# Kernel tuning notes

Hardware: AMD Instinct MI355X
Metric: run time of the kernel (lower is better)

The kernel has to match this reference:

```python
import jax, jax.numpy as jnp
import numpy as np

# GConvLSTM (torch_geometric_temporal) single step, H=None,C=None -> zeros.
# Each gate g uses two ChebConvs: conv_x_g(X) + conv_h_g(H) + (w_c_g*C for i,f; only i,f,o have w_c) + b_g
# With H=C=0: gate preact = conv_x_g(X) + conv_h_g(0) + b_g. ChebConv(0)=0 only if bias=False;
# torch_geometric_temporal ChebConvs use bias=True by default, so conv_h_g(0) = bias_h_g (a vector).
# We fold conv_h bias into b. Cheb recursion with sym norm, lambda_max=2 default in ChebConv? Actually
# ChebConv requires lambda_max or normalization='sym' default uses lambda_max=2.0 assumption:
# Tx_0 = x; Tx_1 = L_hat @ x where L_hat = -D^-1/2 A D^-1/2 (since L_scaled = L - I = -A_norm for lambda_max=2);
# Tx_k = 2*L_hat@Tx_{k-1} - Tx_{k-2}. out = sum_k Tx_k @ W_k + bias.

MULT = 2
IN_CH = 10
WIDTHS = [8 * MULT, 16 * MULT, 32 * MULT, 76 * MULT]
KS = [2, 3, 4, 5]
NUM_CLASSES = 2
N_NODES = 100000
N_EDGES = 3200000


def _norm_adj(edge_index, n):
    src, dst = edge_index[0], edge_index[1]
    deg = jax.ops.segment_sum(jnp.ones_like(src, dtype=jnp.float32), dst, num_segments=n)
    dinv = jnp.where(deg > 0, jax.lax.rsqrt(jnp.maximum(deg, 1.0)), 0.0)
    w = dinv[src] * dinv[dst]  # [E]
    return src, dst, w


def _lhat_mul(x, src, dst, w, n):
    # L_hat @ x = -A_norm @ x  (lambda_max=2, sym norm, no self loops added in scaled L beyond -I cancel)
    msg = x[src] * w[:, None]  # [E,F]
    agg = jax.ops.segment_sum(msg, dst, num_segments=n)
    return -agg


def cheb_conv(x, Ws, b, src, dst, w, n):
    # Ws: [K, F_in, F_out]
    K = Ws.shape[0]
    Tx0 = x
    out = Tx0 @ Ws[0]
    if K > 1:
        Tx1 = _lhat_mul(Tx0, src, dst, w, n)
        out = out + Tx1 @ Ws[1]
        for k in range(2, K):
            Tx2 = 2.0 * _lhat_mul(Tx1, src, dst, w, n) - Tx0
            out = out + Tx2 @ Ws[k]
            Tx0, Tx1 = Tx1, Tx2
    return out + b


def gconv_lstm_step(x, params, src, dst, w, n):
    # params: dict with per-gate Wx,Wh (cheb weights), bx,bh, b, and w_ci,w_cf,w_co
    def conv_pair(g):
        cx = cheb_conv(x, params[f'Wx_{g}'], params[f'bx_{g}'], src, dst, w, n)
        # H = 0 => conv_h contributes only its bias
        return cx + params[f'bh_{g}'] + params[f'b_{g}']
    # C = 0 => peephole terms w_c*C vanish
    i = jax.nn.sigmoid(conv_pair('i'))
    f = jax.nn.sigmoid(conv_pair('f'))
    c = i * jnp.tanh(conv_pair('c'))
    o = jax.nn.sigmoid(conv_pair('o'))
    h = o * jnp.tanh(c)
    return h


def _make_layer_params(key, f_in, f_out, K):
    p = {}
    ks = jax.random.split(key, 16)
    scale = 1.0 / np.sqrt(f_in * K)
    for gi, g in enumerate(['i', 'f', 'c', 'o']):
        p[f'Wx_{g}'] = jax.random.normal(ks[4 * gi], (K, f_in, f_out), jnp.float32) * scale
        p[f'bx_{g}'] = jnp.zeros((f_out,), jnp.float32)
        p[f'bh_{g}'] = jnp.zeros((f_out,), jnp.float32)
        p[f'b_{g}'] = jnp.zeros((f_out,), jnp.float32)
    return p


def setup_inputs() -> dict:
    key = jax.random.key(0)
    kx, ke, kp, kl = jax.random.split(key, 4)
    x = jax.random.normal(kx, (N_NODES, IN_CH), jnp.float32)
    edge_index = jax.random.randint(ke, (2, N_EDGES), 0, N_NODES, dtype=jnp.int64)
    layer_keys = jax.random.split(kp, 4)
    params = []
    f_in = IN_CH
    for li, (f_out, K) in enumerate(zip(WIDTHS, KS)):
        params.append(_make_layer_params(layer_keys[li], f_in, f_out, K))
        f_in = f_out
    flat = {}
    for li, p in enumerate(params):
        for k, v in p.items():
            flat[f'l{li}_{k}'] = v
    kw, kb = jax.random.split(kl)
    flat['lin_W'] = jax.random.normal(kw, (WIDTHS[-1], NUM_CLASSES), jnp.float32) * (1.0 / np.sqrt(WIDTHS[-1]))
    flat['lin_b'] = jnp.zeros((NUM_CLASSES,), jnp.float32)
    return {'x': x, 'edge_index': edge_index, **flat}


_GATE_KEYS = [f'{pre}_{g}' for g in ['i', 'f', 'c', 'o'] for pre in ['Wx', 'bx', 'bh', 'b']]


def _forward(x, edge_index, params_by_layer, lin_W, lin_b):
    n = x.shape[0]
    src, dst, w = _norm_adj(edge_index, n)
    h = x
    for p in params_by_layer:
        h = gconv_lstm_step(h, p, src, dst, w, n)
        h = jax.nn.relu(h)  # dropout: eval mode -> identity
    logits = h @ lin_W + lin_b
    return jax.nn.softmax(logits, axis=-1)


def reference(x, edge_index,
              l0_Wx_i, l0_bx_i, l0_bh_i, l0_b_i, l0_Wx_f, l0_bx_f, l0_bh_f, l0_b_f, l0_Wx_c, l0_bx_c, l0_bh_c, l0_b_c, l0_Wx_o, l0_bx_o, l0_bh_o, l0_b_o,
              l1_Wx_i, l1_bx_i, l1_bh_i, l1_b_i, l1_Wx_f, l1_bx_f, l1_bh_f, l1_b_f, l1_Wx_c, l1_bx_c, l1_bh_c, l1_b_c, l1_Wx_o, l1_bx_o, l1_bh_o, l1_b_o,
              l2_Wx_i, l2_bx_i, l2_bh_i, l2_b_i, l2_Wx_f, l2_bx_f, l2_bh_f, l2_b_f, l2_Wx_c, l2_bx_c, l2_bh_c, l2_b_c, l2_Wx_o, l2_bx_o, l2_bh_o, l2_b_o,
              l3_Wx_i, l3_bx_i, l3_bh_i, l3_b_i, l3_Wx_f, l3_bx_f, l3_bh_f, l3_b_f, l3_Wx_c, l3_bx_c, l3_bh_c, l3_b_c, l3_Wx_o, l3_bx_o, l3_bh_o, l3_b_o,
              lin_W, lin_b):
    loc = locals()
    params_by_layer = []
    for li in range(4):
        params_by_layer.append({k: loc[f'l{li}_{k}'] for k in _GATE_KEYS})
    return _forward(x, edge_index, params_by_layer, lin_W, lin_b)
```

## Files before the change

### kernel.cpp

```cpp
#include <hip/hip_runtime.h>


#define IN_CH 10
typedef unsigned short u16;
typedef unsigned long long u64;
typedef short bf16x8 __attribute__((ext_vector_type(8)));
typedef float f32x4 __attribute__((ext_vector_type(4)));

struct __align__(8) Edge { int s; float w; };

__device__ __forceinline__ float bf2f(u16 u) { return __uint_as_float(((unsigned)u) << 16); }
__device__ __forceinline__ float lo16f(unsigned v) { return __uint_as_float(v << 16); }
__device__ __forceinline__ float hi16f(unsigned v) { return __uint_as_float(v & 0xffff0000u); }
__device__ __forceinline__ u16 f2bf(float f) {
    unsigned x = __float_as_uint(f);
    return (u16)((x + 0x7fff + ((x >> 16) & 1)) >> 16);
}
__device__ __forceinline__ float ldv(const float* p) { return *p; }
__device__ __forceinline__ float ldv(const u16* p) { return bf2f(*p); }
__device__ __forceinline__ void stv(float* p, float v) { *p = v; }
__device__ __forceinline__ void stv(u16* p, float v) { *p = f2bf(v); }


__global__ void k_count(const int* __restrict__ dst, int* __restrict__ cnt, int e) {
    int i = blockIdx.x * 256 + threadIdx.x;
    if (i < e) atomicAdd(&cnt[dst[i]], 1);
}

__global__ void k_dinv(const int* __restrict__ cnt, float* __restrict__ dinv, int n) {
    int i = blockIdx.x * 256 + threadIdx.x;
    if (i < n) dinv[i] = cnt[i] > 0 ? rsqrtf((float)cnt[i]) : 0.f;
}


__global__ void k_bsum(const int* __restrict__ cnt, int* __restrict__ bsum, int n) {
    __shared__ int red[256];
    int t = threadIdx.x;
    int idx = blockIdx.x * 1024 + t * 4;
    int s = 0;
#pragma unroll
    for (int j = 0; j < 4; j++) s += (idx + j < n) ? cnt[idx + j] : 0;
    red[t] = s;
    __syncthreads();
    for (int off = 128; off > 0; off >>= 1) {
        if (t < off) red[t] += red[t + off];
        __syncthreads();
    }
    if (t == 0) bsum[blockIdx.x] = red[0];
}

__global__ __launch_bounds__(1024) void k_bscan(const int* __restrict__ bsum,
                                                int* __restrict__ boff,
                                                int* __restrict__ total_out, int B) {
    __shared__ int sh[1024];
    int t = threadIdx.x;
    int v = t < B ? bsum[t] : 0;
    sh[t] = v;
    __syncthreads();
    for (int off = 1; off < 1024; off <<= 1) {
        int x = (t >= off) ? sh[t - off] : 0;
        __syncthreads();
        sh[t] += x;
        __syncthreads();
    }
    if (t < B) boff[t] = sh[t] - v;
    if (t == B - 1) *total_out = sh[t];
}

__global__ void k_write(const int* __restrict__ cnt, const int* __restrict__ boff,
                        int* __restrict__ row_ptr, int* __restrict__ cursor, int n) {
    __shared__ int tsum[256];
    int t = threadIdx.x;
    int idx = blockIdx.x * 1024 + t * 4;
    int c[4];
    int s = 0;
#pragma unroll
    for (int j = 0; j < 4; j++) {
        c[j] = (idx + j < n) ? cnt[idx + j] : 0;
        s += c[j];
    }
    tsum[t] = s;
    __syncthreads();
    for (int off = 1; off < 256; off <<= 1) {
        int x = (t >= off) ? tsum[t - off] : 0;
        __syncthreads();
        tsum[t] += x;
        __syncthreads();
    }
    int run = boff[blockIdx.x] + tsum[t] - s;
#pragma unroll
    for (int j = 0; j < 4; j++) {
        if (idx + j < n) {
            row_ptr[idx + j] = run;
            cursor[idx + j] = run;
            run += c[j];
        }
    }
}

__global__ void k_fill(const int* __restrict__ src, const int* __restrict__ dst,
                       const float* __restrict__ dinv, int* __restrict__ cursor,
                       Edge* __restrict__ ed, int e, int dlo, int dhi) {
    int i = blockIdx.x * 256 + threadIdx.x;
    if (i >= e) return;
    int d = dst[i];
    if (d < dlo || d >= dhi) return;
    int s = src[i];
    int pos = atomicAdd(&cursor[d], 1);
    float w = dinv[s] * dinv[d];
    u64 v = (u64)(unsigned)s | ((u64)__float_as_uint(w) << 32);
    *(u64*)&ed[pos] = v;
}


template <int F>
__global__ void k_spmv(const u16* __restrict__ X, const u16* __restrict__ Tprev,
                       u16* __restrict__ Tout, const int* __restrict__ row_ptr,
                       const Edge* __restrict__ ed, int n, float scale) {
    int lane = threadIdx.x;
    int node = blockIdx.x * blockDim.y + threadIdx.y;
    if (node >= n) return;
    int lo = row_ptr[node], hi = row_ptr[node + 1];
    const u16* Xc = X + 2 * lane;
    float a0[4] = {0.f, 0.f, 0.f, 0.f};
    float a1[4] = {0.f, 0.f, 0.f, 0.f};
    int e = lo;
    for (; e + 8 <= hi; e += 8) {
        Edge q[8];
#pragma unroll
        for (int j = 0; j < 8; j++) q[j] = ed[e + j];
        unsigned v[8];
#pragma unroll
        for (int j = 0; j < 8; j++)
            v[j] = *(const unsigned*)(Xc + (size_t)q[j].s * F);
#pragma unroll
        for (int j = 0; j < 8; j++) {
            a0[j & 3] = fmaf(q[j].w, lo16f(v[j]), a0[j & 3]);
            a1[j & 3] = fmaf(q[j].w, hi16f(v[j]), a1[j & 3]);
        }
    }
    for (; e + 4 <= hi; e += 4) {
        Edge q[4];
#pragma unroll
        for (int j = 0; j < 4; j++) q[j] = ed[e + j];
        unsigned v[4];
#pragma unroll
        for (int j = 0; j < 4; j++)
            v[j] = *(const unsigned*)(Xc + (size_t)q[j].s * F);
#pragma unroll
        for (int j = 0; j < 4; j++) {
            a0[j] = fmaf(q[j].w, lo16f(v[j]), a0[j]);
            a1[j] = fmaf(q[j].w, hi16f(v[j]), a1[j]);
        }
    }
    for (; e < hi; e++) {
        Edge q = ed[e];
        unsigned v = *(const unsigned*)(Xc + (size_t)q.s * F);
        a0[0] = fmaf(q.w, lo16f(v), a0[0]);
        a1[0] = fmaf(q.w, hi16f(v), a1[0]);
    }
    float v0 = -scale * ((a0[0] + a0[1]) + (a0[2] + a0[3]));
    float v1 = -scale * ((a1[0] + a1[1]) + (a1[2] + a1[3]));
    if (Tprev) {
        unsigned pv = *(const unsigned*)(Tprev + (size_t)node * F + 2 * lane);
        v0 -= lo16f(pv);
        v1 -= hi16f(pv);
    }
    *(unsigned*)(Tout + (size_t)node * F + 2 * lane) =
        (unsigned)f2bf(v0) | ((unsigned)f2bf(v1) << 16);
}

struct TP { const void* p[5]; };

template <typename ST, int FIN, int K>
__global__ __launch_bounds__(256) void k_chebgate(TP tp, const float* __restrict__ Wp,
                                                  const float* __restrict__ b4,
                                                  ST* __restrict__ H, int n, int F,
                                                  int F4pad) {
    __shared__ float As[FIN][68];
    __shared__ float Ws[FIN][128];
    const int tid = threadIdx.x;
    const int fx = tid & 31, ry = tid >> 5;
    const int row0 = blockIdx.y * 64;
    const int f0 = blockIdx.x * 32;
    const int f = f0 + fx;

    float acc[8][3];
    const float4 bv = *(const float4*)&b4[(size_t)f * 4];
#pragma unroll
    for (int r = 0; r < 8; r++) { acc[r][0] = bv.x; acc[r][1] = bv.y; acc[r][2] = bv.z; }

#pragma unroll
    for (int t = 0; t < K; t++) {
        const ST* T = (const ST*)tp.p[t];
        for (int idx = tid; idx < 64 * FIN; idx += 256) {
            int r = idx / FIN, a = idx - r * FIN;
            int rr = row0 + r;
            if (rr >= n) rr = n - 1;
            As[a][r] = ldv(&T[(size_t)rr * FIN + a]);
        }
        const float* Wt = Wp + (size_t)t * FIN * F4pad + (size_t)f0 * 4;
        for (int idx = tid; idx < FIN * 128; idx += 256) {
            int aa = idx >> 7, c = idx & 127;
            Ws[aa][c] = Wt[(size_t)aa * F4pad + c];
        }
        __syncthreads();
#pragma unroll 2
        for (int a = 0; a < FIN; a++) {
            const float4 w = *(const float4*)&Ws[a][fx * 4];
            const float4 x0 = *(const float4*)&As[a][ry * 8];
            const float4 x1 = *(const float4*)&As[a][ry * 8 + 4];
            const float xr[8] = {x0.x, x0.y, x0.z, x0.w, x1.x, x1.y, x1.z, x1.w};
#pragma unroll
            for (int r = 0; r < 8; r++) {
                acc[r][0] = fmaf(xr[r], w.x, acc[r][0]);
                acc[r][1] = fmaf(xr[r], w.y, acc[r][1]);
                acc[r][2] = fmaf(xr[r], w.z, acc[r][2]);
            }
        }
        __syncthreads();
    }

    if (f < F) {
#pragma unroll
        for (int r = 0; r < 8; r++) {
            int row = row0 + ry * 8 + r;
            if (row < n) {
                float gi = 1.f / (1.f + __expf(-acc[r][0]));
                float go = 1.f / (1.f + __expf(-acc[r][2]));
                float c = gi * tanhf(acc[r][1]);
                float h = go * tanhf(c);
                stv(&H[(size_t)row * F + f], fmaxf(h, 0.f));
            }
        }
    }
}


template <int FIN, int K, int FPAD, int NT>
__global__ __launch_bounds__(256) void k_chebgate_mfma(TP tp, const u16* __restrict__ Wt,
                                                       const float* __restrict__ b3,
                                                       u16* __restrict__ H, int n, int F,
                                                       int Hstride) {
    constexpr int KT = K * FIN;
    const int xb = blockIdx.x / NT;
    const int yb = blockIdx.x % NT;
    const int wave = threadIdx.x >> 6;
    const int lane = threadIdx.x & 63;
    const int r0 = xb * 128 + wave * 32;
    const int f0 = yb * 32;
    const int ln = lane & 15;
    const int lk = lane >> 4;

    f32x4 acc[2][2][3];
#pragma unroll
    for (int rt = 0; rt < 2; rt++)
#pragma unroll
        for (int s = 0; s < 2; s++)
#pragma unroll
            for (int g = 0; g < 3; g++) acc[rt][s][g] = (f32x4){0.f, 0.f, 0.f, 0.f};

    int arow[2];
#pragma unroll
    for (int rt = 0; rt < 2; rt++) {
        int row = r0 + rt * 16 + ln;
        arow[rt] = row < n ? row : n - 1;
    }

    for (int k0 = 0; k0 < KT; k0 += 32) {
        const int t = k0 / FIN;
        const int a0 = k0 % FIN;
        const u16* T = (const u16*)tp.p[t];
        bf16x8 af[2];
#pragma unroll
        for (int rt = 0; rt < 2; rt++)
            af[rt] = *(const bf16x8*)(T + (size_t)arow[rt] * FIN + a0 + lk * 8);
#pragma unroll
        for (int s = 0; s < 2; s++) {
#pragma unroll
            for (int g = 0; g < 3; g++) {
                int col = g * FPAD + f0 + s * 16 + ln;
                bf16x8 bf = *(const bf16x8*)(Wt + (size_t)col * KT + k0 + lk * 8);
#pragma unroll
                for (int rt = 0; rt < 2; rt++)
                    acc[rt][s][g] = __builtin_amdgcn_mfma_f32_16x16x32_bf16(
                        af[rt], bf, acc[rt][s][g], 0, 0, 0);
            }
        }
    }

#pragma unroll
    for (int s = 0; s < 2; s++) {
        int fcol = f0 + s * 16 + ln;
        if (fcol >= F) continue;
        float bi = b3[0 * FPAD + fcol];
        float bc = b3[1 * FPAD + fcol];
        float bo = b3[2 * FPAD + fcol];
#pragma unroll
        for (int rt = 0; rt < 2; rt++) {
#pragma unroll
            for (int reg = 0; reg < 4; reg++) {
                int row = r0 + rt * 16 + lk * 4 + reg;
                if (row < n) {
                    float gi = 1.f / (1.f + __expf(-(acc[rt][s][0][reg] + bi)));
                    float go = 1.f / (1.f + __expf(-(acc[rt][s][2][reg] + bo)));
                    float c = gi * tanhf(acc[rt][s][1][reg] + bc);
                    float h = go * tanhf(c);
                    H[(size_t)row * Hstride + fcol] = f2bf(fmaxf(h, 0.f));
                }
            }
        }
    }
}


template <int FIN, int K, int FPAD, int NT>
__global__ __launch_bounds__(256) void k_chebgate_mfma_fused(
    TP tp, const u16* __restrict__ Wt, const float* __restrict__ b3,
    const float* __restrict__ W2, float* __restrict__ part, int n, int F) {
    constexpr int KT = K * FIN;
    const int xb = blockIdx.x / NT;
    const int yb = blockIdx.x % NT;
    const int wave = threadIdx.x >> 6;
    const int lane = threadIdx.x & 63;
    const int r0 = xb * 128 + wave * 32;
    const int f0 = yb * 32;
    const int ln = lane & 15;
    const int lk = lane >> 4;

    f32x4 acc[2][2][3];
#pragma unroll
    for (int rt = 0; rt < 2; rt++)
#pragma unroll
        for (int s = 0; s < 2; s++)
#pragma unroll
            for (int g = 0; g < 3; g++) acc[rt][s][g] = (f32x4){0.f, 0.f, 0.f, 0.f};

    int arow[2];
#pragma unroll
    for (int rt = 0; rt < 2; rt++) {
        int row = r0 + rt * 16 + ln;
        arow[rt] = row < n ? row : n - 1;
    }

    for (int k0 = 0; k0 < KT; k0 += 32) {
        const int t = k0 / FIN;
        const int a0 = k0 % FIN;
        const u16* T = (const u16*)tp.p[t];
        bf16x8 af[2];
#pragma unroll
        for (int rt = 0; rt < 2; rt++)
            af[rt] = *(const bf16x8*)(T + (size_t)arow[rt] * FIN + a0 + lk * 8);
#pragma unroll
        for (int s = 0; s < 2; s++) {
#pragma unroll
            for (int g = 0; g < 3; g++) {
                int col = g * FPAD + f0 + s * 16 + ln;
                bf16x8 bf = *(const bf16x8*)(Wt + (size_t)col * KT + k0 + lk * 8);
#pragma unroll
                for (int rt = 0; rt < 2; rt++)
                    acc[rt][s][g] = __builtin_amdgcn_mfma_f32_16x16x32_bf16(
                        af[rt], bf, acc[rt][s][g], 0, 0, 0);
            }
        }
    }

    float p0[2][4], p1[2][4];
#pragma unroll
    for (int rt = 0; rt < 2; rt++)
#pragma unroll
        for (int reg = 0; reg < 4; reg++) { p0[rt][reg] = 0.f; p1[rt][reg] = 0.f; }

#pragma unroll
    for (int s = 0; s < 2; s++) {
        int fcol = f0 + s * 16 + ln;
        float w20 = fcol < F ? W2[fcol * 2 + 0] : 0.f;
        float w21 = fcol < F ? W2[fcol * 2 + 1] : 0.f;
        float bi = b3[0 * FPAD + fcol];
        float bc = b3[1 * FPAD + fcol];
        float bo = b3[2 * FPAD + fcol];
#pragma unroll
        for (int rt = 0; rt < 2; rt++) {
#pragma unroll
            for (int reg = 0; reg < 4; reg++) {
                float gi = 1.f / (1.f + __expf(-(acc[rt][s][0][reg] + bi)));
                float go = 1.f / (1.f + __expf(-(acc[rt][s][2][reg] + bo)));
                float c = gi * tanhf(acc[rt][s][1][reg] + bc);
                float h = fmaxf(go * tanhf(c), 0.f);
                p0[rt][reg] = fmaf(h, w20, p0[rt][reg]);
                p1[rt][reg] = fmaf(h, w21, p1[rt][reg]);
            }
        }
    }

#pragma unroll
    for (int rt = 0; rt < 2; rt++) {
#pragma unroll
        for (int reg = 0; reg < 4; reg++) {
            float v0 = p0[rt][reg], v1 = p1[rt][reg];
#pragma unroll
            for (int m = 1; m <= 8; m <<= 1) {
                v0 += __shfl_xor(v0, m);
                v1 += __shfl_xor(v1, m);
            }
            p0[rt][reg] = v0;
            p1[rt][reg] = v1;
        }
    }

    if (ln == 0) {
#pragma unroll
        for (int rt = 0; rt < 2; rt++) {
#pragma unroll
            for (int reg = 0; reg < 4; reg++) {
                int row = r0 + rt * 16 + lk * 4 + reg;
                if (row < n) {
                    float* pp = part + ((size_t)yb * n + row) * 2;
                    pp[0] = p0[rt][reg];
                    pp[1] = p1[rt][reg];
                }
            }
        }
    }
}

__global__ void k_smax(const float* __restrict__ part, const float* __restrict__ b,
                       float* __restrict__ out, int n, int ntiles) {
    int i = blockIdx.x * 256 + threadIdx.x;
    if (i >= n) return;
    float l0 = b[0], l1 = b[1];
    for (int t = 0; t < ntiles; t++) {
        const float* pp = part + ((size_t)t * n + i) * 2;
        l0 += pp[0];
        l1 += pp[1];
    }
    float m = fmaxf(l0, l1);
    float e0 = __expf(l0 - m), e1 = __expf(l1 - m);
    float s = 1.f / (e0 + e1);
    out[(size_t)i * 2 + 0] = e0 * s;
    out[(size_t)i * 2 + 1] = e1 * s;
}


__global__ void k_pack_w(const float* __restrict__ Wi, const float* __restrict__ Wc,
                         const float* __restrict__ Wo, float* __restrict__ Wp,
                         int KFIN, int F, int F4pad) {
    int idx = blockIdx.x * 256 + threadIdx.x;
    int tot = KFIN * F4pad;
    if (idx >= tot) return;
    int c = idx % F4pad;
    int ka = idx / F4pad;
    int f = c >> 2, g = c & 3;
    float v = 0.f;
    if (g < 3 && f < F) {
        const float* Wg = (g == 0) ? Wi : ((g == 1) ? Wc : Wo);
        v = Wg[(size_t)ka * F + f];
    }
    Wp[idx] = v;
}

__global__ void k_pack_b(const float* __restrict__ bxi, const float* __restrict__ bhi,
                         const float* __restrict__ bi, const float* __restrict__ bxc,
                         const float* __restrict__ bhc, const float* __restrict__ bc,
                         const float* __restrict__ bxo, const float* __restrict__ bho,
                         const float* __restrict__ bo, float* __restrict__ b4,
                         int F, int F4pad) {
    int idx = blockIdx.x * 256 + threadIdx.x;
    if (idx >= F4pad) return;
    int f = idx >> 2, g = idx & 3;
    float v = 0.f;
    if (g < 3 && f < F) {
        if (g == 0) v = bxi[f] + bhi[f] + bi[f];
        else if (g == 1) v = bxc[f] + bhc[f] + bc[f];
        else v = bxo[f] + bho[f] + bo[f];
    }
    b4[idx] = v;
}

__global__ void k_pack_wt(const float* __restrict__ Wi, const float* __restrict__ Wc,
                          const float* __restrict__ Wo, u16* __restrict__ Wt,
                          int KT, int Fin, int F, int FPAD) {
    int idx = blockIdx.x * 256 + threadIdx.x;
    int tot = 3 * FPAD * KT;
    if (idx >= tot) return;
    int k = idx % KT;
    int col = idx / KT;
    int g = col / FPAD, f = col % FPAD;
    int t = k / Fin, a = k % Fin;
    float v = 0.f;
    if (f < F) {
        const float* Wg = (g == 0) ? Wi : ((g == 1) ? Wc : Wo);
        v = Wg[((size_t)t * Fin + a) * F + f];
    }
    Wt[idx] = f2bf(v);
}

__global__ void k_pack_b3(const float* __restrict__ bxi, const float* __restrict__ bhi,
                          const float* __restrict__ bi, const float* __restrict__ bxc,
                          const float* __restrict__ bhc, const float* __restrict__ bc,
                          const float* __restrict__ bxo, const float* __restrict__ bho,
                          const float* __restrict__ bo, float* __restrict__ b3,
                          int F, int FPAD) {
    int idx = blockIdx.x * 256 + threadIdx.x;
    if (idx >= 3 * FPAD) return;
    int g = idx / FPAD, f = idx % FPAD;
    float v = 0.f;
    if (f < F) {
        if (g == 0) v = bxi[f] + bhi[f] + bi[f];
        else if (g == 1) v = bxc[f] + bhc[f] + bc[f];
        else v = bxo[f] + bho[f] + bo[f];
    }
    b3[idx] = v;
}

__global__ void k_cvt(const float* __restrict__ x, u16* __restrict__ y, int n) {
    int i = blockIdx.x * 256 + threadIdx.x;
    if (i < n) y[i] = f2bf(x[i]);
}


static inline size_t al(size_t x) { return (x + 255) & ~(size_t)255; }

extern "C" void kernel_launch(void* const* d_in, const int* in_sizes, int n_in,
                              void* d_out, int out_size, void* d_ws, size_t ws_size,
                              hipStream_t stream) {
    const float* X0 = (const float*)d_in[0];
    const int* ei = (const int*)d_in[1];
    const int N = in_sizes[0] / IN_CH;
    const int E = in_sizes[1] / 2;
    const int* src = ei;
    const int* dst = ei + E;

    char* p = (char*)d_ws;
    size_t off = 0;
    auto carve = [&](size_t bytes) -> char* { char* r = p + off; off += al(bytes); return r; };
    int* row_ptr  = (int*)carve((size_t)(N + 1) * 4);
    int* cnt      = (int*)carve((size_t)N * 4);
    int* cursor   = (int*)carve((size_t)N * 4);
    float* dinv   = (float*)carve((size_t)N * 4);
    int* bsum     = (int*)carve((size_t)1024 * 4);
    int* boff     = (int*)carve((size_t)1024 * 4);
    Edge* edges   = (Edge*)carve((size_t)E * 8);
    const size_t S64 = al((size_t)N * 64 * 2);
    char* bufA    = carve(5 * S64);
    char* bufB    = carve((size_t)N * 304);
    float* Wp     = (float*)carve((size_t)48 * 128 * 4);
    float* b4     = (float*)carve((size_t)128 * 4);
    u16* Wt       = (u16*)carve((size_t)480 * 320 * 2);
    float* b3     = (float*)carve((size_t)480 * 4);
    (void)ws_size;

    u16* X0c  = (u16*)bufA;
    u16* T0_1 = (u16*)(bufA + al((size_t)N * 20));
    u16* H0   = (u16*)(bufA + S64);
    u16* T1_1 = (u16*)(bufA + S64 + al((size_t)N * 32));
    u16* T1_2 = (u16*)(bufA + S64 + 2 * al((size_t)N * 32));
    u16* L2T[4];
    for (int t = 0; t < 4; t++) L2T[t] = (u16*)(bufB + t * al((size_t)N * 64));
    u16* L3T[5];
    for (int t = 0; t < 5; t++) L3T[t] = (u16*)(bufA + t * S64);
    float* part = (float*)bufB;

    int gE = (E + 255) / 256, gN = (N + 255) / 256;
    int B = (N + 1023) / 1024;
    hipMemsetAsync(cnt, 0, (size_t)N * 4, stream);
    k_count<<<gE, 256, 0, stream>>>(dst, cnt, E);
    k_dinv<<<gN, 256, 0, stream>>>(cnt, dinv, N);
    k_bsum<<<B, 256, 0, stream>>>(cnt, bsum, N);
    k_bscan<<<1, 1024, 0, stream>>>(bsum, boff, row_ptr + N, B);
    k_write<<<B, 256, 0, stream>>>(cnt, boff, row_ptr, cursor, N);
    const int NB = 8;
    for (int b = 0; b < NB; b++) {
        int dlo = (int)((long long)N * b / NB);
        int dhi = (int)((long long)N * (b + 1) / NB);
        k_fill<<<gE, 256, 0, stream>>>(src, dst, dinv, cursor, edges, E, dlo, dhi);
    }

    k_cvt<<<(N * IN_CH + 255) / 256, 256, 0, stream>>>(X0, X0c, N * IN_CH);

    dim3 gv(1, (N + 63) / 64);
    int rb = (N + 127) / 128;

    dim3 bs5(5, 48);   int g5 = (N + 47) / 48;
    dim3 bs8(8, 32);   int g8 = (N + 31) / 32;
    dim3 bs16(16, 16); int g16 = (N + 15) / 16;
    dim3 bs32(32, 8);  int g32 = (N + 7) / 8;

    {
        k_pack_w<<<(20 * 128 + 255) / 256, 256, 0, stream>>>(
            (const float*)d_in[2], (const float*)d_in[10], (const float*)d_in[14], Wp, 20, 16, 128);
        k_pack_b<<<1, 256, 0, stream>>>(
            (const float*)d_in[3], (const float*)d_in[4], (const float*)d_in[5],
            (const float*)d_in[11], (const float*)d_in[12], (const float*)d_in[13],
            (const float*)d_in[15], (const float*)d_in[16], (const float*)d_in[17], b4, 16, 128);
        k_spmv<10><<<g5, bs5, 0, stream>>>(X0c, nullptr, T0_1, row_ptr, edges, N, 1.f);
        TP tp; tp.p[0] = X0c; tp.p[1] = T0_1;
        k_chebgate<u16, 10, 2><<<gv, 256, 0, stream>>>(tp, Wp, b4, H0, N, 16, 128);
    }
    {
        k_pack_w<<<(48 * 128 + 255) / 256, 256, 0, stream>>>(
            (const float*)d_in[18], (const float*)d_in[26], (const float*)d_in[30], Wp, 48, 32, 128);
        k_pack_b<<<1, 256, 0, stream>>>(
            (const float*)d_in[19], (const float*)d_in[20], (const float*)d_in[21],
            (const float*)d_in[27], (const float*)d_in[28], (const float*)d_in[29],
            (const float*)d_in[31], (const float*)d_in[32], (const float*)d_in[33], b4, 32, 128);
        k_spmv<16><<<g8, bs8, 0, stream>>>(H0, nullptr, T1_1, row_ptr, edges, N, 1.f);
        k_spmv<16><<<g8, bs8, 0, stream>>>(T1_1, H0, T1_2, row_ptr, edges, N, 2.f);
        TP tp; tp.p[0] = H0; tp.p[1] = T1_1; tp.p[2] = T1_2;
        k_chebgate<u16, 16, 3><<<gv, 256, 0, stream>>>(tp, Wp, b4, L2T[0], N, 32, 128);
    }
    {
        k_pack_wt<<<(3 * 64 * 128 + 255) / 256, 256, 0, stream>>>(
            (const float*)d_in[34], (const float*)d_in[42], (const float*)d_in[46], Wt, 128, 32, 64, 64);
        k_pack_b3<<<1, 256, 0, stream>>>(
            (const float*)d_in[35], (const float*)d_in[36], (const float*)d_in[37],
            (const float*)d_in[43], (const float*)d_in[44], (const float*)d_in[45],
            (const float*)d_in[47], (const float*)d_in[48], (const float*)d_in[49], b3, 64, 64);
        k_spmv<32><<<g16, bs16, 0, stream>>>(L2T[0], nullptr, L2T[1], row_ptr, edges, N, 1.f);
        k_spmv<32><<<g16, bs16, 0, stream>>>(L2T[1], L2T[0], L2T[2], row_ptr, edges, N, 2.f);
        k_spmv<32><<<g16, bs16, 0, stream>>>(L2T[2], L2T[1], L2T[3], row_ptr, edges, N, 2.f);
        TP tp; for (int t = 0; t < 4; t++) tp.p[t] = L2T[t];
        k_chebgate_mfma<32, 4, 64, 2><<<rb * 2, 256, 0, stream>>>(tp, Wt, b3, L3T[0], N, 64, 64);
    }
    {
        k_pack_wt<<<(3 * 160 * 320 + 255) / 256, 256, 0, stream>>>(
            (const float*)d_in[50], (const float*)d_in[58], (const float*)d_in[62], Wt, 320, 64, 152, 160);
        k_pack_b3<<<2, 256, 0, stream>>>(
            (const float*)d_in[51], (const float*)d_in[52], (const float*)d_in[53],
            (const float*)d_in[59], (const float*)d_in[60], (const float*)d_in[61],
            (const float*)d_in[63], (const float*)d_in[64], (const float*)d_in[65], b3, 152, 160);
        k_spmv<64><<<g32, bs32, 0, stream>>>(L3T[0], nullptr, L3T[1], row_ptr, edges, N, 1.f);
        k_spmv<64><<<g32, bs32, 0, stream>>>(L3T[1], L3T[0], L3T[2], row_ptr, edges, N, 2.f);
        k_spmv<64><<<g32, bs32, 0, stream>>>(L3T[2], L3T[1], L3T[3], row_ptr, edges, N, 2.f);
        k_spmv<64><<<g32, bs32, 0, stream>>>(L3T[3], L3T[2], L3T[4], row_ptr, edges, N, 2.f);
        TP tp; for (int t = 0; t < 5; t++) tp.p[t] = L3T[t];
        k_chebgate_mfma_fused<64, 5, 160, 5><<<rb * 5, 256, 0, stream>>>(
            tp, Wt, b3, (const float*)d_in[66], part, N, 152);
    }

    k_smax<<<gN, 256, 0, stream>>>(part, (const float*)d_in[67], (float*)d_out, N, 5);
}
```

Measured before the change: 1.236 ms.

## Stage Chebyshev A panels in LDS and loop over output tiles per block

The MFMA gate kernels now load each block's 128-row panel of all K Chebyshev terms into LDS once with global_load_lds and an XOR swizzle. Each block then loops over all output column tiles, where before one block was launched per (row block, column tile). Weights are pre-packed into MFMA fragment order so each lane reads contiguous 16 bytes. This removes redundant global reads of the A operand across column tiles. The cost is large LDS use (up to 80KB for layer 3), which limits occupancy, and fewer blocks in flight.

```diff
diff --git a/kernel.cpp b/kernel.cpp
--- a/kernel.cpp
+++ b/kernel.cpp
@@ -20,6 +20,12 @@
 __device__ __forceinline__ float ldv(const u16* p) { return bf2f(*p); }
 __device__ __forceinline__ void stv(float* p, float v) { *p = v; }
 __device__ __forceinline__ void stv(u16* p, float v) { *p = f2bf(v); }
+
+__device__ __forceinline__ void gload16(const u16* g, u16* l) {
+    __builtin_amdgcn_global_load_lds(
+        (const __attribute__((address_space(1))) unsigned*)(const void*)g,
+        (__attribute__((address_space(3))) unsigned*)(void*)l, 16, 0, 0);
+}
 
 
 __global__ void k_count(const int* __restrict__ dst, int* __restrict__ cnt, int e) {
@@ -237,187 +243,229 @@
 }
 
 
-template <int FIN, int K, int FPAD, int NT>
-__global__ __launch_bounds__(256) void k_chebgate_mfma(TP tp, const u16* __restrict__ Wt,
-                                                       const float* __restrict__ b3,
-                                                       u16* __restrict__ H, int n, int F,
-                                                       int Hstride) {
-    constexpr int KT = K * FIN;
-    const int xb = blockIdx.x / NT;
-    const int yb = blockIdx.x % NT;
-    const int wave = threadIdx.x >> 6;
-    const int lane = threadIdx.x & 63;
-    const int r0 = xb * 128 + wave * 32;
-    const int f0 = yb * 32;
-    const int ln = lane & 15;
-    const int lk = lane >> 4;
-
-    f32x4 acc[2][2][3];
-#pragma unroll
-    for (int rt = 0; rt < 2; rt++)
-#pragma unroll
-        for (int s = 0; s < 2; s++)
-#pragma unroll
-            for (int g = 0; g < 3; g++) acc[rt][s][g] = (f32x4){0.f, 0.f, 0.f, 0.f};
-
-    int arow[2];
-#pragma unroll
-    for (int rt = 0; rt < 2; rt++) {
-        int row = r0 + rt * 16 + ln;
-        arow[rt] = row < n ? row : n - 1;
-    }
-
-    for (int k0 = 0; k0 < KT; k0 += 32) {
-        const int t = k0 / FIN;
-        const int a0 = k0 % FIN;
-        const u16* T = (const u16*)tp.p[t];
-        bf16x8 af[2];
+template <int FIN, int K, int NT, int FPAD>
+__global__ __launch_bounds__(256) void k_chebgate_mfma2(TP tp, const u16* __restrict__ Bp,
+                                                        const float* __restrict__ b3,
+                                                        u16* __restrict__ H, int n, int F,
+                                                        int Hstride) {
+    constexpr int NIT = K * FIN / 32;
+    constexpr int CPR = FIN / 8;
+    constexpr int CSH = (CPR == 8) ? 3 : 2;
+    constexpr int PANEL = 128 * FIN;
+    constexpr int IPT = (128 * CPR) / 256;
+    __shared__ __align__(16) u16 Alds[K * PANEL];
+
+    const int tid = threadIdx.x;
+    const int xb = blockIdx.x;
+    const int wv = tid >> 6, lane = tid & 63;
+    const int ln = lane & 15, lk = lane >> 4;
+    const size_t panel_g = (size_t)xb * 128 * FIN;
+
+#pragma unroll
+    for (int t = 0; t < K; t++) {
+        const u16* g = (const u16*)tp.p[t] + panel_g;
+#pragma unroll
+        for (int i = 0; i < IPT; i++) {
+            int j0 = wv * (IPT * 64) + i * 64;
+            int j = j0 + lane;
+            int row = j >> CSH, c = j & (CPR - 1);
+            int sc = (j & ~(CPR - 1)) | (c ^ (row & (CPR - 1)));
+            gload16(g + (size_t)sc * 8, Alds + (size_t)t * PANEL + (size_t)j0 * 8);
+        }
+    }
+    __syncthreads();
+
+    const int r0 = xb * 128 + wv * 32;
+    const u16* Bl = Bp + (size_t)lane * 8;
+
+#pragma unroll 1
+    for (int yb = 0; yb < NT; yb++) {
+        f32x4 acc[2][2][3];
 #pragma unroll
         for (int rt = 0; rt < 2; rt++)
-            af[rt] = *(const bf16x8*)(T + (size_t)arow[rt] * FIN + a0 + lk * 8);
+#pragma unroll
+            for (int s = 0; s < 2; s++)
+#pragma unroll
+                for (int g = 0; g < 3; g++) acc[rt][s][g] = (f32x4){0.f, 0.f, 0.f, 0.f};
+
+#pragma unroll
+        for (int it = 0; it < NIT; it++) {
+            const int k0 = it * 32;
+            const int t = k0 / FIN;
+            const int a0 = k0 % FIN;
+            bf16x8 af[2];
+#pragma unroll
+            for (int rt = 0; rt < 2; rt++) {
+                int lrow = wv * 32 + rt * 16 + ln;
+                int kc = (a0 >> 3) + lk;
+                int kcs = kc ^ (lrow & (CPR - 1));
+                af[rt] = *(const bf16x8*)(Alds + (size_t)t * PANEL + (size_t)lrow * FIN + kcs * 8);
+            }
+#pragma unroll
+            for (int s = 0; s < 2; s++)
+#pragma unroll
+                for (int g = 0; g < 3; g++) {
+                    int fi = (yb * NIT + it) * 6 + s * 3 + g;
+                    bf16x8 bf = *(const bf16x8*)(Bl + (size_t)fi * 512);
+#pragma unroll
+                    for (int rt = 0; rt < 2; rt++)
+                        acc[rt][s][g] = __builtin_amdgcn_mfma_f32_16x16x32_bf16(
+                            af[rt], bf, acc[rt][s][g], 0, 0, 0);
+                }
+        }
+
+        const int f0 = yb * 32;
 #pragma unroll
         for (int s = 0; s < 2; s++) {
-#pragma unroll
-            for (int g = 0; g < 3; g++) {
-                int col = g * FPAD + f0 + s * 16 + ln;
-                bf16x8 bf = *(const bf16x8*)(Wt + (size_t)col * KT + k0 + lk * 8);
-#pragma unroll
-                for (int rt = 0; rt < 2; rt++)
-                    acc[rt][s][g] = __builtin_amdgcn_mfma_f32_16x16x32_bf16(
-                        af[rt], bf, acc[rt][s][g], 0, 0, 0);
-            }
-        }
-    }
-
-#pragma unroll
-    for (int s = 0; s < 2; s++) {
-        int fcol = f0 + s * 16 + ln;
-        if (fcol >= F) continue;
-        float bi = b3[0 * FPAD + fcol];
-        float bc = b3[1 * FPAD + fcol];
-        float bo = b3[2 * FPAD + fcol];
-#pragma unroll
-        for (int rt = 0; rt < 2; rt++) {
-#pragma unroll
-            for (int reg = 0; reg < 4; reg++) {
-                int row = r0 + rt * 16 + lk * 4 + reg;
-                if (row < n) {
+            int fcol = f0 + s * 16 + ln;
+            if (fcol >= F) continue;
+            float bi = b3[0 * FPAD + fcol];
+            float bc = b3[1 * FPAD + fcol];
+            float bo = b3[2 * FPAD + fcol];
+#pragma unroll
+            for (int rt = 0; rt < 2; rt++) {
+#pragma unroll
+                for (int reg = 0; reg < 4; reg++) {
+                    int row = r0 + rt * 16 + lk * 4 + reg;
+                    if (row < n) {
+                        float gi = 1.f / (1.f + __expf(-(acc[rt][s][0][reg] + bi)));
+                        float go = 1.f / (1.f + __expf(-(acc[rt][s][2][reg] + bo)));
+                        float c = gi * tanhf(acc[rt][s][1][reg] + bc);
+                        float h = go * tanhf(c);
+                        H[(size_t)row * Hstride + fcol] = f2bf(fmaxf(h, 0.f));
+                    }
+                }
+            }
+        }
+    }
+}
+
+
+template <int FIN, int K, int NT, int FPAD>
+__global__ __launch_bounds__(256) void k_chebgate_mfma_fused2(
+    TP tp, const u16* __restrict__ Bp, const float* __restrict__ b3,
+    const float* __restrict__ W2, float* __restrict__ part, int n, int F) {
+    constexpr int NIT = K * FIN / 32;
+    constexpr int CPR = FIN / 8;
+    constexpr int CSH = (CPR == 8) ? 3 : 2;
+    constexpr int PANEL = 128 * FIN;
+    constexpr int IPT = (128 * CPR) / 256;
+    __shared__ __align__(16) u16 Alds[K * PANEL];
+
+    const int tid = threadIdx.x;
+    const int xb = blockIdx.x;
+    const int wv = tid >> 6, lane = tid & 63;
+    const int ln = lane & 15, lk = lane >> 4;
+    const size_t panel_g = (size_t)xb * 128 * FIN;
+
+#pragma unroll
+    for (int t = 0; t < K; t++) {
+        const u16* g = (const u16*)tp.p[t] + panel_g;
+#pragma unroll
+        for (int i = 0; i < IPT; i++) {
+            int j0 = wv * (IPT * 64) + i * 64;
+            int j = j0 + lane;
+            int row = j >> CSH, c = j & (CPR - 1);
+            int sc = (j & ~(CPR - 1)) | (c ^ (row & (CPR - 1)));
+            gload16(g + (size_t)sc * 8, Alds + (size_t)t * PANEL + (size_t)j0 * 8);
+        }
+    }
+    __syncthreads();
+
+    const int r0 = xb * 128 + wv * 32;
+    const u16* Bl = Bp + (size_t)lane * 8;
+
+#pragma unroll 1
+    for (int yb = 0; yb < NT; yb++) {
+        f32x4 acc[2][2][3];
+#pragma unroll
+        for (int rt = 0; rt < 2; rt++)
+#pragma unroll
+            for (int s = 0; s < 2; s++)
+#pragma unroll
+                for (int g = 0; g < 3; g++) acc[rt][s][g] = (f32x4){0.f, 0.f, 0.f, 0.f};
+
+#pragma unroll
+        for (int it = 0; it < NIT; it++) {
+            const int k0 = it * 32;
+            const int t = k0 / FIN;
+            const int a0 = k0 % FIN;
+            bf16x8 af[2];
+#pragma unroll
+            for (int rt = 0; rt < 2; rt++) {
+                int lrow = wv * 32 + rt * 16 + ln;
+                int kc = (a0 >> 3) + lk;
+                int kcs = kc ^ (lrow & (CPR - 1));
+                af[rt] = *(const bf16x8*)(Alds + (size_t)t * PANEL + (size_t)lrow * FIN + kcs * 8);
+            }
+#pragma unroll
+            for (int s = 0; s < 2; s++)
+#pragma unroll
+                for (int g = 0; g < 3; g++) {
+                    int fi = (yb * NIT + it) * 6 + s * 3 + g;
+                    bf16x8 bf = *(const bf16x8*)(Bl + (size_t)fi * 512);
+#pragma unroll
+                    for (int rt = 0; rt < 2; rt++)
+                        acc[rt][s][g] = __builtin_amdgcn_mfma_f32_16x16x32_bf16(
+                            af[rt], bf, acc[rt][s][g], 0, 0, 0);
+                }
+        }
+
+        const int f0 = yb * 32;
+        float p0[2][4], p1[2][4];
+#pragma unroll
+        for (int rt = 0; rt < 2; rt++)
+#pragma unroll
+            for (int reg = 0; reg < 4; reg++) { p0[rt][reg] = 0.f; p1[rt][reg] = 0.f; }
+
+#pragma unroll
+        for (int s = 0; s < 2; s++) {
+            int fcol = f0 + s * 16 + ln;
+            float w20 = fcol < F ? W2[fcol * 2 + 0] : 0.f;
+            float w21 = fcol < F ? W2[fcol * 2 + 1] : 0.f;
+            float bi = b3[0 * FPAD + fcol];
+            float bc = b3[1 * FPAD + fcol];
+            float bo = b3[2 * FPAD + fcol];
+#pragma unroll
+            for (int rt = 0; rt < 2; rt++) {
+#pragma unroll
+                for (int reg = 0; reg < 4; reg++) {
                     float gi = 1.f / (1.f + __expf(-(acc[rt][s][0][reg] + bi)));
                     float go = 1.f / (1.f + __expf(-(acc[rt][s][2][reg] + bo)));
                     float c = gi * tanhf(acc[rt][s][1][reg] + bc);
-                    float h = go * tanhf(c);
-                    H[(size_t)row * Hstride + fcol] = f2bf(fmaxf(h, 0.f));
+                    float h = fmaxf(go * tanhf(c), 0.f);
+                    p0[rt][reg] = fmaf(h, w20, p0[rt][reg]);
+                    p1[rt][reg] = fmaf(h, w21, p1[rt][reg]);
                 }
             }
         }
-    }
-}
-
-
-template <int FIN, int K, int FPAD, int NT>
-__global__ __launch_bounds__(256) void k_chebgate_mfma_fused(
-    TP tp, const u16* __restrict__ Wt, const float* __restrict__ b3,
-    const float* __restrict__ W2, float* __restrict__ part, int n, int F) {
-    constexpr int KT = K * FIN;
-    const int xb = blockIdx.x / NT;
-    const int yb = blockIdx.x % NT;
-    const int wave = threadIdx.x >> 6;
-    const int lane = threadIdx.x & 63;
-    const int r0 = xb * 128 + wave * 32;
-    const int f0 = yb * 32;
-    const int ln = lane & 15;
-    const int lk = lane >> 4;
-
-    f32x4 acc[2][2][3];
-#pragma unroll
-    for (int rt = 0; rt < 2; rt++)
-#pragma unroll
-        for (int s = 0; s < 2; s++)
-#pragma unroll
-            for (int g = 0; g < 3; g++) acc[rt][s][g] = (f32x4){0.f, 0.f, 0.f, 0.f};
-
-    int arow[2];
-#pragma unroll
-    for (int rt = 0; rt < 2; rt++) {
-        int row = r0 + rt * 16 + ln;
-        arow[rt] = row < n ? row : n - 1;
-    }
-
-    for (int k0 = 0; k0 < KT; k0 += 32) {
-        const int t = k0 / FIN;
-        const int a0 = k0 % FIN;
-        const u16* T = (const u16*)tp.p[t];
-        bf16x8 af[2];
-#pragma unroll
-        for (int rt = 0; rt < 2; rt++)
-            af[rt] = *(const bf16x8*)(T + (size_t)arow[rt] * FIN + a0 + lk * 8);
-#pragma unroll
-        for (int s = 0; s < 2; s++) {
-#pragma unroll
-            for (int g = 0; g < 3; g++) {
-                int col = g * FPAD + f0 + s * 16 + ln;
-                bf16x8 bf = *(const bf16x8*)(Wt + (size_t)col * KT + k0 + lk * 8);
-#pragma unroll
-                for (int rt = 0; rt < 2; rt++)
-                    acc[rt][s][g] = __builtin_amdgcn_mfma_f32_16x16x32_bf16(
-                        af[rt], bf, acc[rt][s][g], 0, 0, 0);
-            }
-        }
-    }
-
-    float p0[2][4], p1[2][4];
-#pragma unroll
-    for (int rt = 0; rt < 2; rt++)
-#pragma unroll
-        for (int reg = 0; reg < 4; reg++) { p0[rt][reg] = 0.f; p1[rt][reg] = 0.f; }
-
-#pragma unroll
-    for (int s = 0; s < 2; s++) {
-        int fcol = f0 + s * 16 + ln;
-        float w20 = fcol < F ? W2[fcol * 2 + 0] : 0.f;
-        float w21 = fcol < F ? W2[fcol * 2 + 1] : 0.f;
-        float bi = b3[0 * FPAD + fcol];
-        float bc = b3[1 * FPAD + fcol];
-        float bo = b3[2 * FPAD + fcol];
+
 #pragma unroll
         for (int rt = 0; rt < 2; rt++) {
 #pragma unroll
             for (int reg = 0; reg < 4; reg++) {
-                float gi = 1.f / (1.f + __expf(-(acc[rt][s][0][reg] + bi)));
-                float go = 1.f / (1.f + __expf(-(acc[rt][s][2][reg] + bo)));
-                float c = gi * tanhf(acc[rt][s][1][reg] + bc);
-                float h = fmaxf(go * tanhf(c), 0.f);
-                p0[rt][reg] = fmaf(h, w20, p0[rt][reg]);
-                p1[rt][reg] = fmaf(h, w21, p1[rt][reg]);
-            }
-        }
-    }
-
-#pragma unroll
-    for (int rt = 0; rt < 2; rt++) {
-#pragma unroll
-        for (int reg = 0; reg < 4; reg++) {
-            float v0 = p0[rt][reg], v1 = p1[rt][reg];
-#pragma unroll
-            for (int m = 1; m <= 8; m <<= 1) {
-                v0 += __shfl_xor(v0, m);
-                v1 += __shfl_xor(v1, m);
-            }
-            p0[rt][reg] = v0;
-            p1[rt][reg] = v1;
-        }
-    }
-
-    if (ln == 0) {
-#pragma unroll
-        for (int rt = 0; rt < 2; rt++) {
-#pragma unroll
-            for (int reg = 0; reg < 4; reg++) {
-                int row = r0 + rt * 16 + lk * 4 + reg;
-                if (row < n) {
-                    float* pp = part + ((size_t)yb * n + row) * 2;
-                    pp[0] = p0[rt][reg];
-                    pp[1] = p1[rt][reg];
+                float v0 = p0[rt][reg], v1 = p1[rt][reg];
+#pragma unroll
+                for (int m = 1; m <= 8; m <<= 1) {
+                    v0 += __shfl_xor(v0, m);
+                    v1 += __shfl_xor(v1, m);
+                }
+                p0[rt][reg] = v0;
+                p1[rt][reg] = v1;
+            }
+        }
+
+        if (ln == 0) {
+#pragma unroll
+            for (int rt = 0; rt < 2; rt++) {
+#pragma unroll
+                for (int reg = 0; reg < 4; reg++) {
+                    int row = r0 + rt * 16 + lk * 4 + reg;
+                    if (row < n) {
+                        float* pp = part + ((size_t)yb * n + row) * 2;
+                        pp[0] = p0[rt][reg];
+                        pp[1] = p1[rt][reg];
+                    }
                 }
             }
         }
@@ -477,22 +525,29 @@
     b4[idx] = v;
 }
 
-__global__ void k_pack_wt(const float* __restrict__ Wi, const float* __restrict__ Wc,
-                          const float* __restrict__ Wo, u16* __restrict__ Wt,
-                          int KT, int Fin, int F, int FPAD) {
+__global__ void k_pack_wf(const float* __restrict__ Wi, const float* __restrict__ Wc,
+                          const float* __restrict__ Wo, u16* __restrict__ Bp,
+                          int NIT, int Fin, int F, int NT) {
     int idx = blockIdx.x * 256 + threadIdx.x;
-    int tot = 3 * FPAD * KT;
+    int tot = NT * NIT * 6 * 512;
     if (idx >= tot) return;
-    int k = idx % KT;
-    int col = idx / KT;
-    int g = col / FPAD, f = col % FPAD;
+    int frag = idx >> 9;
+    int r = idx & 511;
+    int lane = r >> 3, j = r & 7;
+    int lk = lane >> 4, ln = lane & 15;
+    int yb = frag / (NIT * 6);
+    int q = frag % (NIT * 6);
+    int it = q / 6, sg = q % 6;
+    int s = sg / 3, g = sg % 3;
+    int fcol = yb * 32 + s * 16 + ln;
+    int k = it * 32 + lk * 8 + j;
     int t = k / Fin, a = k % Fin;
     float v = 0.f;
-    if (f < F) {
+    if (fcol < F) {
         const float* Wg = (g == 0) ? Wi : ((g == 1) ? Wc : Wo);
-        v = Wg[((size_t)t * Fin + a) * F + f];
-    }
-    Wt[idx] = f2bf(v);
+        v = Wg[((size_t)t * Fin + a) * F + fcol];
+    }
+    Bp[idx] = f2bf(v);
 }
 
 __global__ void k_pack_b3(const float* __restrict__ bxi, const float* __restrict__ bhi,
@@ -610,8 +665,8 @@
         k_chebgate<u16, 16, 3><<<gv, 256, 0, stream>>>(tp, Wp, b4, L2T[0], N, 32, 128);
     }
     {
-        k_pack_wt<<<(3 * 64 * 128 + 255) / 256, 256, 0, stream>>>(
-            (const float*)d_in[34], (const float*)d_in[42], (const float*)d_in[46], Wt, 128, 32, 64, 64);
+        k_pack_wf<<<(2 * 4 * 6 * 512 + 255) / 256, 256, 0, stream>>>(
+            (const float*)d_in[34], (const float*)d_in[42], (const float*)d_in[46], Wt, 4, 32, 64, 2);
         k_pack_b3<<<1, 256, 0, stream>>>(
             (const float*)d_in[35], (const float*)d_in[36], (const float*)d_in[37],
             (const float*)d_in[43], (const float*)d_in[44], (const float*)d_in[45],
@@ -620,11 +675,11 @@
         k_spmv<32><<<g16, bs16, 0, stream>>>(L2T[1], L2T[0], L2T[2], row_ptr, edges, N, 2.f);
         k_spmv<32><<<g16, bs16, 0, stream>>>(L2T[2], L2T[1], L2T[3], row_ptr, edges, N, 2.f);
         TP tp; for (int t = 0; t < 4; t++) tp.p[t] = L2T[t];
-        k_chebgate_mfma<32, 4, 64, 2><<<rb * 2, 256, 0, stream>>>(tp, Wt, b3, L3T[0], N, 64, 64);
+        k_chebgate_mfma2<32, 4, 2, 64><<<rb, 256, 0, stream>>>(tp, Wt, b3, L3T[0], N, 64, 64);
     }
     {
-        k_pack_wt<<<(3 * 160 * 320 + 255) / 256, 256, 0, stream>>>(
-            (const float*)d_in[50], (const float*)d_in[58], (const float*)d_in[62], Wt, 320, 64, 152, 160);
+        k_pack_wf<<<(5 * 10 * 6 * 512 + 255) / 256, 256, 0, stream>>>(
+            (const float*)d_in[50], (const float*)d_in[58], (const float*)d_in[62], Wt, 10, 64, 152, 5);
         k_pack_b3<<<2, 256, 0, stream>>>(
             (const float*)d_in[51], (const float*)d_in[52], (const float*)d_in[53],
             (const float*)d_in[59], (const float*)d_in[60], (const float*)d_in[61],
@@ -634,7 +689,7 @@
         k_spmv<64><<<g32, bs32, 0, stream>>>(L3T[2], L3T[1], L3T[3], row_ptr, edges, N, 2.f);
         k_spmv<64><<<g32, bs32, 0, stream>>>(L3T[3], L3T[2], L3T[4], row_ptr, edges, N, 2.f);
         TP tp; for (int t = 0; t < 5; t++) tp.p[t] = L3T[t];
-        k_chebgate_mfma_fused<64, 5, 160, 5><<<rb * 5, 256, 0, stream>>>(
+        k_chebgate_mfma_fused2<64, 5, 5, 160><<<rb, 256, 0, stream>>>(
             tp, Wt, b3, (const float*)d_in[66], part, N, 152);
     }
 
```

New measurement: 1.182 ms. 4.4% less time.
